# Performance work log

Measured on AMD Instinct MI355X. Metric: run time of the kernel, lower is better.

## Reference

```python
import jax, jax.numpy as jnp
import numpy as np

COMMITMENT_COST = 0.25
NUM_EMBEDDINGS = 4096
EMBEDDING_DIM = 256


def setup_inputs() -> dict:
    key = jax.random.key(0)
    kx, ke = jax.random.split(key)
    x = jax.random.normal(kx, (64, 1024, EMBEDDING_DIM), dtype=jnp.float32)
    # nn.Embedding weight initialized uniform(-1/K, 1/K)
    emb = jax.random.uniform(ke, (NUM_EMBEDDINGS, EMBEDDING_DIM), dtype=jnp.float32,
                             minval=-1.0 / NUM_EMBEDDINGS, maxval=1.0 / NUM_EMBEDDINGS)
    return {"x": x, "emb": emb}


def reference(x, emb):
    D = emb.shape[1]
    flat_x = x.reshape(-1, D)                                    # [N, D]
    distances = (jnp.sum(flat_x * flat_x, axis=1, keepdims=True)
                 - 2.0 * flat_x @ emb.T
                 + jnp.sum(emb * emb, axis=1))
    indices = jnp.argmin(distances, axis=1)                      # [N]
    quantized = emb[indices].reshape(x.shape)                    # [..., D]
    e_latent_loss = jnp.mean((jax.lax.stop_gradient(quantized) - x) ** 2)
    q_latent_loss = jnp.mean((quantized - jax.lax.stop_gradient(x)) ** 2)
    loss = q_latent_loss + COMMITMENT_COST * e_latent_loss
    # straight-through estimator
    quantized = x + jax.lax.stop_gradient(quantized - x)
    return quantized, loss, indices[:, None]
```

## Files before the change

kernel.cpp:

```cpp
#include <hip/hip_runtime.h>
#include <math.h>

#define DIMD 256
#define KCODES 4096
#define NROWS 65536
#define QN (NROWS * DIMD)

constexpr int P1_BM = 64;
constexpr int P1_BN = 128;
constexpr int NT    = KCODES / P1_BN;
constexpr int NCHUNK = NT * 2;
constexpr float TAU2 = 7.5e-4f;
constexpr float TAU2B = TAU2 + 1e-5f;
constexpr int CAP   = 48;
constexpr int NS    = 8;

typedef __attribute__((ext_vector_type(8))) short bf16x8;
typedef __attribute__((ext_vector_type(4))) float f32x4;

#define VM8() asm volatile("s_waitcnt vmcnt(8)" ::: "memory")
#define VM0() asm volatile("s_waitcnt vmcnt(0)" ::: "memory")

__device__ __forceinline__ unsigned short f2bf(float f) {
    unsigned int u = __builtin_bit_cast(unsigned int, f);
    u += 0x7fffu + ((u >> 16) & 1u);
    return (unsigned short)(u >> 16);
}

__device__ __forceinline__ float opaque(float v) {
    asm volatile("" : "+v"(v));
    return v;
}

__device__ __forceinline__ void gload_lds16(const void* g, void* l) {
    __builtin_amdgcn_global_load_lds(
        (const __attribute__((address_space(1))) unsigned int*)g,
        (__attribute__((address_space(3))) unsigned int*)l, 16, 0, 0);
}

__global__ void sx_kernel(const float* __restrict__ x, float* __restrict__ sx) {
    const int j   = threadIdx.x & 7;
    const int row = blockIdx.x * 32 + (threadIdx.x >> 3);
    const float* p = x + (size_t)row * DIMD;
    float total = 0.0f;
    #pragma unroll
    for (int half = 0; half < 2; ++half) {
        const float* b = p + half * 128;
        const float v0 = b[j];
        float r = opaque(v0 * v0);
        #pragma unroll
        for (int i = 8; i < 128; i += 8) {
            const float v = b[i + j];
            r += opaque(v * v);
        }
        const float s1  = r  + __shfl_xor(r, 1, 64);
        const float s2  = s1 + __shfl_xor(s1, 2, 64);
        const float res = s2 + __shfl_xor(s2, 4, 64);
        total = (half == 0) ? res : (total + res);
    }
    if (j == 0) sx[row] = total;
}

__global__ void se_kernel(const float* __restrict__ emb, float* __restrict__ se) {
    const int j   = threadIdx.x & 7;
    const int row = blockIdx.x * 32 + (threadIdx.x >> 3);
    const float* p = emb + (size_t)row * DIMD;
    float total = 0.0f;
    #pragma unroll
    for (int half = 0; half < 2; ++half) {
        const float* b = p + half * 128;
        const float v0 = b[j];
        float r = opaque(v0 * v0);
        #pragma unroll
        for (int i = 8; i < 128; i += 8) {
            const float v = b[i + j];
            r += opaque(v * v);
        }
        const float s1  = r  + __shfl_xor(r, 1, 64);
        const float s2  = s1 + __shfl_xor(s1, 2, 64);
        const float res = s2 + __shfl_xor(s2, 4, 64);
        total = (half == 0) ? res : (total + res);
    }
    if (j == 0) se[row] = total;
}

__global__ void conv_emb_kernel(const float* __restrict__ emb, unsigned short* __restrict__ embh) {
    const int i = blockIdx.x * blockDim.x + threadIdx.x;
    const float4 v = ((const float4*)emb)[i];
    ushort4 h;
    h.x = f2bf(v.x); h.y = f2bf(v.y); h.z = f2bf(v.z); h.w = f2bf(v.w);
    ((ushort4*)embh)[i] = h;
}

__global__ __launch_bounds__(256, 2)
void pass1_kernel(const float* __restrict__ x, const unsigned short* __restrict__ embh,
                  unsigned int* __restrict__ cand, int* __restrict__ cnt_out) {
    __shared__ unsigned short Bs[2][16384];
    __shared__ unsigned int cand_lds[P1_BM * CAP];
    __shared__ float part[4][32];
    __shared__ float tilemax[P1_BM];
    __shared__ int   cnts[P1_BM];

    const int t    = threadIdx.x;
    const int w    = t >> 6;
    const int lane = t & 63;
    const int quad = lane >> 4;
    const int lm   = lane & 15;
    const int wr   = w >> 1;
    const int wc   = w & 1;
    const int row0 = blockIdx.x * P1_BM;

    if (t < P1_BM) cnts[t] = 0;

    bf16x8 afr[2][8];
    #pragma unroll
    for (int f = 0; f < 2; ++f) {
        const float* xr = x + (size_t)(row0 + wr * 32 + f * 16 + lm) * DIMD + quad * 8;
        #pragma unroll
        for (int c = 0; c < 8; ++c) {
            const float4 v0 = *(const float4*)(xr + c * 32);
            const float4 v1 = *(const float4*)(xr + c * 32 + 4);
            bf16x8 h;
            h[0] = (short)f2bf(v0.x); h[1] = (short)f2bf(v0.y);
            h[2] = (short)f2bf(v0.z); h[3] = (short)f2bf(v0.w);
            h[4] = (short)f2bf(v1.x); h[5] = (short)f2bf(v1.y);
            h[6] = (short)f2bf(v1.z); h[7] = (short)f2bf(v1.w);
            afr[f][c] = h;
        }
    }

    auto stage = [&](int buf, int m) {
        const int c0  = (m >> 1) * P1_BN;
        const int kcb = (m & 1) * 128;
        #pragma unroll
        for (int i = 0; i < 8; ++i) {
            const int seg = i * 4 + w;
            const int c   = seg * 4 + (lane >> 4);
            const int kk  = ((lane & 15) ^ (c & 15)) * 8;
            const unsigned short* src = embh + (size_t)(c0 + c) * DIMD + kcb + kk;
            gload_lds16(src, &Bs[buf][seg * 512]);
        }
    };

    stage(0, 0);
    int buf = 0;

    float rmg[2][4];
    #pragma unroll
    for (int f = 0; f < 2; ++f)
        #pragma unroll
        for (int reg = 0; reg < 4; ++reg) rmg[f][reg] = -INFINITY;

    for (int tile = 0; tile < NT; ++tile) {
        const int c0 = tile * P1_BN;
        f32x4 acc[2][4];
        #pragma unroll
        for (int f = 0; f < 2; ++f)
            #pragma unroll
            for (int g = 0; g < 4; ++g) acc[f][g] = (f32x4){0.f, 0.f, 0.f, 0.f};

        #pragma unroll
        for (int kb = 0; kb < 2; ++kb) {
            const int m = tile * 2 + kb;
            __syncthreads();
            if (m + 1 < NCHUNK) {
                stage(buf ^ 1, m + 1);
                VM8();
            } else {
                VM0();
            }
            __syncthreads();

            #pragma unroll
            for (int ks = 0; ks < 4; ++ks) {
                bf16x8 b[4];
                #pragma unroll
                for (int g = 0; g < 4; ++g) {
                    const int c = wc * 64 + g * 16 + lm;
                    b[g] = *(const bf16x8*)
                        &Bs[buf][c * 128 + ((((ks << 2) + quad) ^ lm) << 3)];
                }
                #pragma unroll
                for (int f = 0; f < 2; ++f)
                    #pragma unroll
                    for (int g = 0; g < 4; ++g)
                        acc[f][g] = __builtin_amdgcn_mfma_f32_16x16x32_bf16(
                            afr[f][kb * 4 + ks], b[g], acc[f][g], 0, 0, 0);
            }
            buf ^= 1;
        }

        #pragma unroll
        for (int f = 0; f < 2; ++f) {
            f32x4 mm4;
            #pragma unroll
            for (int reg = 0; reg < 4; ++reg) {
                float mm = fmaxf(fmaxf(acc[f][0][reg], acc[f][1][reg]),
                                 fmaxf(acc[f][2][reg], acc[f][3][reg]));
                #pragma unroll
                for (int off = 1; off < 16; off <<= 1)
                    mm = fmaxf(mm, __shfl_xor(mm, off, 64));
                mm4[reg] = mm;
            }
            if (lm == 0)
                *(f32x4*)&part[w][f * 16 + quad * 4] = mm4;
        }

        __syncthreads();
        if (t < P1_BM) {
            const int trg = t >> 5, loc = t & 31;
            tilemax[t] = fmaxf(part[trg * 2][loc], part[trg * 2 + 1][loc]);
        }
        __syncthreads();

        #pragma unroll
        for (int f = 0; f < 2; ++f) {
            const f32x4 tm = *(const f32x4*)&tilemax[wr * 32 + f * 16 + quad * 4];
            #pragma unroll
            for (int reg = 0; reg < 4; ++reg) {
                rmg[f][reg] = fmaxf(rmg[f][reg], tm[reg]);
                const float thr = rmg[f][reg] - TAU2;
                const int r = wr * 32 + f * 16 + quad * 4 + reg;
                #pragma unroll
                for (int g = 0; g < 4; ++g) {
                    const float dv = acc[f][g][reg];
                    if (dv > thr) {
                        const int slot = atomicAdd(&cnts[r], 1);
                        if (slot < CAP) {
                            const unsigned int ub =
                                __builtin_bit_cast(unsigned int, fmaxf(dv, 0.0f));
                            cand_lds[r * CAP + slot] =
                                (ub & 0xFFFFF000u) |
                                (unsigned int)(c0 + wc * 64 + g * 16 + lm);
                        }
                    }
                }
            }
        }
    }
    __syncthreads();

    {
        const uint4* src = (const uint4*)cand_lds;
        uint4* dst = (uint4*)(cand + (size_t)row0 * CAP);
        #pragma unroll
        for (int i = 0; i < P1_BM * CAP / 4 / 256; ++i)
            dst[i * 256 + t] = src[i * 256 + t];
    }
    if (t < P1_BM) cnt_out[row0 + t] = (cnts[t] > CAP) ? -1 : cnts[t];
}

__global__ __launch_bounds__(256, 4)
void pass2_kernel(const float* __restrict__ x, const float* __restrict__ emb,
                  const float* __restrict__ sx, const float* __restrict__ se,
                  const unsigned int* __restrict__ cand, const int* __restrict__ cnt,
                  float* __restrict__ out, float* __restrict__ partial) {
    __shared__ float4 xsh[4][64];
    __shared__ float4 esh[4][NS][64];
    const int w = threadIdx.x >> 6, lane = threadIdx.x & 63;
    const int row = blockIdx.x * 4 + w;
    const int n = cnt[row];
    const unsigned int word = cand[(size_t)row * CAP + lane];
    const float sxr = sx[row];
    const float4 myx = ((const float4*)(x + (size_t)row * DIMD))[lane];
    const float4* emb4 = (const float4*)emb;

    xsh[w][lane] = myx;
    const float4* xs4 = &xsh[w][0];

    float bestd = INFINITY;
    int   bestc = 0x7fffffff;
    int   wslot = 0x7fffffff;

    if (n >= 1 && n <= CAP) {
        const float dtil = (lane < n)
            ? __builtin_bit_cast(float, word & 0xFFFFF000u) : -INFINITY;
        const int code = (int)(word & 0xFFFu);
        float mx = dtil;
        #pragma unroll
        for (int off = 1; off < 64; off <<= 1)
            mx = fmaxf(mx, __shfl_xor(mx, off, 64));
        const bool active = (lane < n) && (dtil > mx - TAU2B);
        const unsigned long long mask = __ballot(active);
        const int nact = __popcll(mask);
        const int slot = __popcll(mask & ((1ull << lane) - 1ull));
        unsigned long long mm = mask;
        const int ns = nact < NS ? nact : NS;
        for (int i = 0; i < ns; ++i) {
            const int li = __ffsll(mm) - 1;
            mm &= mm - 1;
            const int bc = __shfl(code, li, 64);
            gload_lds16(emb4 + (size_t)bc * 64 + lane, &esh[w][i][0]);
        }
        VM0();
        if (active) {
            float a = 0.0f;
            if (slot < NS) {
                const float4* ep4 = &esh[w][slot][0];
                #pragma unroll
                for (int d4 = 0; d4 < DIMD / 4; ++d4) {
                    const float4 ev = ep4[d4];
                    const float4 xv = xs4[d4];
                    a = fmaf(xv.x, ev.x, a);
                    a = fmaf(xv.y, ev.y, a);
                    a = fmaf(xv.z, ev.z, a);
                    a = fmaf(xv.w, ev.w, a);
                }
            } else {
                const float4* ep4 = emb4 + (size_t)code * 64;
                #pragma unroll
                for (int d4 = 0; d4 < DIMD / 4; ++d4) {
                    const float4 ev = ep4[d4];
                    const float4 xv = xs4[d4];
                    a = fmaf(xv.x, ev.x, a);
                    a = fmaf(xv.y, ev.y, a);
                    a = fmaf(xv.z, ev.z, a);
                    a = fmaf(xv.w, ev.w, a);
                }
            }
            const float t1 = sxr - 2.0f * a;
            bestd = t1 + se[code];
            bestc = code;
            wslot = slot;
        }
    } else {
        for (int c = lane; c < KCODES; c += 64) {
            const float* ep = emb + (size_t)c * DIMD;
            float a = 0.0f;
            for (int d4 = 0; d4 < DIMD / 4; ++d4) {
                const float4 xv = xs4[d4];
                const float4 ev = ((const float4*)ep)[d4];
                a = fmaf(xv.x, ev.x, a);
                a = fmaf(xv.y, ev.y, a);
                a = fmaf(xv.z, ev.z, a);
                a = fmaf(xv.w, ev.w, a);
            }
            const float t1 = sxr - 2.0f * a;
            const float dd = t1 + se[c];
            if (dd < bestd || (dd == bestd && c < bestc)) { bestd = dd; bestc = c; }
        }
    }
    #pragma unroll
    for (int off = 32; off > 0; off >>= 1) {
        const float od = __shfl_down(bestd, off, 64);
        const int   oc = __shfl_down(bestc, off, 64);
        const int   os = __shfl_down(wslot, off, 64);
        if (od < bestd || (od == bestd && oc < bestc)) {
            bestd = od; bestc = oc; wslot = os;
        }
    }
    bestc = __shfl(bestc, 0, 64);
    wslot = __shfl(wslot, 0, 64);

    const float4 e4 = (wslot < NS) ? esh[w][wslot][lane]
                                   : emb4[(size_t)bestc * 64 + lane];
    ((float4*)(out + (size_t)row * DIMD))[lane] = e4;
    const float dx = e4.x - myx.x, dy = e4.y - myx.y,
                dz = e4.z - myx.z, dw = e4.w - myx.w;
    float s = dx * dx + dy * dy + dz * dz + dw * dw;
    #pragma unroll
    for (int off = 32; off > 0; off >>= 1) s += __shfl_down(s, off, 64);
    if (lane == 0) {
        partial[row] = s;
        out[QN + 1 + row] = (float)bestc;
    }
}

__global__ void loss_reduce_kernel(const float* __restrict__ partial, float* __restrict__ out) {
    const int t = threadIdx.x;
    double s = 0.0;
    for (int i = t; i < NROWS; i += 256) s += (double)partial[i];
    __shared__ double tsum[256];
    tsum[t] = s;
    __syncthreads();
    #pragma unroll
    for (int off = 128; off > 0; off >>= 1) {
        if (t < off) tsum[t] += tsum[t + off];
        __syncthreads();
    }
    if (t == 0) out[QN] = (float)(tsum[0] * (1.25 / (double)QN));
}

extern "C" void kernel_launch(void* const* d_in, const int* in_sizes, int n_in,
                              void* d_out, int out_size, void* d_ws, size_t ws_size,
                              hipStream_t stream) {
    const float* x   = (const float*)d_in[0];
    const float* emb = (const float*)d_in[1];
    float* out = (float*)d_out;

    char* ws = (char*)d_ws;
    unsigned short* embh = (unsigned short*)ws;           ws += (size_t)KCODES * DIMD * 2;
    float* sx  = (float*)ws;                              ws += (size_t)NROWS * 4;
    float* se  = (float*)ws;                              ws += (size_t)KCODES * 4;
    unsigned int* cand = (unsigned int*)ws;               ws += (size_t)NROWS * CAP * 4;
    int*   cnt  = (int*)ws;                               ws += (size_t)NROWS * 4;
    float* partial = (float*)ws;

    conv_emb_kernel<<<KCODES * DIMD / 4 / 256, 256, 0, stream>>>(emb, embh);
    sx_kernel<<<NROWS / 32, 256, 0, stream>>>(x, sx);
    se_kernel<<<KCODES / 32, 256, 0, stream>>>(emb, se);
    pass1_kernel<<<NROWS / P1_BM, 256, 0, stream>>>(x, embh, cand, cnt);
    pass2_kernel<<<NROWS / 4, 256, 0, stream>>>(x, emb, sx, se, cand, cnt, out, partial);
    loss_reduce_kernel<<<1, 256, 0, stream>>>(partial, out);
}
```

Before: 744.0 us.

## Make pass2 waves process four rows with next-row prefetch and single-candidate shortcut

```diff
diff --git a/kernel.cpp b/kernel.cpp
--- a/kernel.cpp
+++ b/kernel.cpp
@@ -13,7 +13,8 @@
 constexpr float TAU2 = 7.5e-4f;
 constexpr float TAU2B = TAU2 + 1e-5f;
 constexpr int CAP   = 48;
-constexpr int NS    = 8;
+constexpr int NS    = 6;
+constexpr int P2_WAVES = 16384;
 
 typedef __attribute__((ext_vector_type(8))) short bf16x8;
 typedef __attribute__((ext_vector_type(4))) float f32x4;
@@ -256,113 +257,140 @@
                   const unsigned int* __restrict__ cand, const int* __restrict__ cnt,
                   float* __restrict__ out, float* __restrict__ partial) {
     __shared__ float4 xsh[4][64];
-    __shared__ float4 esh[4][NS][64];
+    __shared__ float4 esh[4][NS][65];
     const int w = threadIdx.x >> 6, lane = threadIdx.x & 63;
-    const int row = blockIdx.x * 4 + w;
-    const int n = cnt[row];
-    const unsigned int word = cand[(size_t)row * CAP + lane];
-    const float sxr = sx[row];
-    const float4 myx = ((const float4*)(x + (size_t)row * DIMD))[lane];
+    const int wid = blockIdx.x * 4 + w;
     const float4* emb4 = (const float4*)emb;
 
-    xsh[w][lane] = myx;
-    const float4* xs4 = &xsh[w][0];
-
-    float bestd = INFINITY;
-    int   bestc = 0x7fffffff;
-    int   wslot = 0x7fffffff;
-
-    if (n >= 1 && n <= CAP) {
-        const float dtil = (lane < n)
-            ? __builtin_bit_cast(float, word & 0xFFFFF000u) : -INFINITY;
-        const int code = (int)(word & 0xFFFu);
-        float mx = dtil;
-        #pragma unroll
-        for (int off = 1; off < 64; off <<= 1)
-            mx = fmaxf(mx, __shfl_xor(mx, off, 64));
-        const bool active = (lane < n) && (dtil > mx - TAU2B);
-        const unsigned long long mask = __ballot(active);
-        const int nact = __popcll(mask);
-        const int slot = __popcll(mask & ((1ull << lane) - 1ull));
-        unsigned long long mm = mask;
-        const int ns = nact < NS ? nact : NS;
-        for (int i = 0; i < ns; ++i) {
-            const int li = __ffsll(mm) - 1;
-            mm &= mm - 1;
-            const int bc = __shfl(code, li, 64);
-            gload_lds16(emb4 + (size_t)bc * 64 + lane, &esh[w][i][0]);
-        }
-        VM0();
-        if (active) {
-            float a = 0.0f;
-            if (slot < NS) {
-                const float4* ep4 = &esh[w][slot][0];
-                #pragma unroll
+    int          n    = cnt[wid];
+    unsigned int word = cand[(size_t)wid * CAP + lane];
+    float        sxr  = sx[wid];
+    float4       myx  = ((const float4*)(x + (size_t)wid * DIMD))[lane];
+
+    #pragma unroll
+    for (int r = 0; r < 4; ++r) {
+        const int row = wid + r * P2_WAVES;
+
+        int n2 = 0; unsigned int word2 = 0; float sxr2 = 0.0f; float4 myx2{};
+        if (r < 3) {
+            const int rn = wid + (r + 1) * P2_WAVES;
+            n2    = cnt[rn];
+            word2 = cand[(size_t)rn * CAP + lane];
+            sxr2  = sx[rn];
+            myx2  = ((const float4*)(x + (size_t)rn * DIMD))[lane];
+        }
+
+        xsh[w][lane] = myx;
+        const float4* xs4 = &xsh[w][0];
+
+        float bestd = INFINITY;
+        int   bestc = 0x7fffffff;
+        int   wslot = 0x7fffffff;
+        bool  fast  = false;
+
+        if (n >= 1 && n <= CAP) {
+            const float dtil = (lane < n)
+                ? __builtin_bit_cast(float, word & 0xFFFFF000u) : -INFINITY;
+            const int code = (int)(word & 0xFFFu);
+            float mx = dtil;
+            #pragma unroll
+            for (int off = 1; off < 64; off <<= 1)
+                mx = fmaxf(mx, __shfl_xor(mx, off, 64));
+            const bool active = (lane < n) && (dtil > mx - TAU2B);
+            const unsigned long long mask = __ballot(active);
+            const int nact = __popcll(mask);
+            if (nact == 1) {
+                const int li = __ffsll(mask) - 1;
+                bestc = __shfl(code, li, 64);
+                fast  = true;
+            } else {
+                const int slot = __popcll(mask & ((1ull << lane) - 1ull));
+                unsigned long long mm = mask;
+                const int ns = nact < NS ? nact : NS;
+                for (int i = 0; i < ns; ++i) {
+                    const int li = __ffsll(mm) - 1;
+                    mm &= mm - 1;
+                    const int bc = __shfl(code, li, 64);
+                    gload_lds16(emb4 + (size_t)bc * 64 + lane, &esh[w][i][0]);
+                }
+                VM0();
+                if (active) {
+                    float a = 0.0f;
+                    if (slot < NS) {
+                        const float4* ep4 = &esh[w][slot][0];
+                        #pragma unroll
+                        for (int d4 = 0; d4 < DIMD / 4; ++d4) {
+                            const float4 ev = ep4[d4];
+                            const float4 xv = xs4[d4];
+                            a = fmaf(xv.x, ev.x, a);
+                            a = fmaf(xv.y, ev.y, a);
+                            a = fmaf(xv.z, ev.z, a);
+                            a = fmaf(xv.w, ev.w, a);
+                        }
+                    } else {
+                        const float4* ep4 = emb4 + (size_t)code * 64;
+                        #pragma unroll
+                        for (int d4 = 0; d4 < DIMD / 4; ++d4) {
+                            const float4 ev = ep4[d4];
+                            const float4 xv = xs4[d4];
+                            a = fmaf(xv.x, ev.x, a);
+                            a = fmaf(xv.y, ev.y, a);
+                            a = fmaf(xv.z, ev.z, a);
+                            a = fmaf(xv.w, ev.w, a);
+                        }
+                    }
+                    const float t1 = sxr - 2.0f * a;
+                    bestd = t1 + se[code];
+                    bestc = code;
+                    wslot = slot;
+                }
+            }
+        } else {
+            for (int c = lane; c < KCODES; c += 64) {
+                const float* ep = emb + (size_t)c * DIMD;
+                float a = 0.0f;
                 for (int d4 = 0; d4 < DIMD / 4; ++d4) {
-                    const float4 ev = ep4[d4];
                     const float4 xv = xs4[d4];
+                    const float4 ev = ((const float4*)ep)[d4];
                     a = fmaf(xv.x, ev.x, a);
                     a = fmaf(xv.y, ev.y, a);
                     a = fmaf(xv.z, ev.z, a);
                     a = fmaf(xv.w, ev.w, a);
                 }
-            } else {
-                const float4* ep4 = emb4 + (size_t)code * 64;
-                #pragma unroll
-                for (int d4 = 0; d4 < DIMD / 4; ++d4) {
-                    const float4 ev = ep4[d4];
-                    const float4 xv = xs4[d4];
-                    a = fmaf(xv.x, ev.x, a);
-                    a = fmaf(xv.y, ev.y, a);
-                    a = fmaf(xv.z, ev.z, a);
-                    a = fmaf(xv.w, ev.w, a);
-                }
-            }
-            const float t1 = sxr - 2.0f * a;
-            bestd = t1 + se[code];
-            bestc = code;
-            wslot = slot;
-        }
-    } else {
-        for (int c = lane; c < KCODES; c += 64) {
-            const float* ep = emb + (size_t)c * DIMD;
-            float a = 0.0f;
-            for (int d4 = 0; d4 < DIMD / 4; ++d4) {
-                const float4 xv = xs4[d4];
-                const float4 ev = ((const float4*)ep)[d4];
-                a = fmaf(xv.x, ev.x, a);
-                a = fmaf(xv.y, ev.y, a);
-                a = fmaf(xv.z, ev.z, a);
-                a = fmaf(xv.w, ev.w, a);
-            }
-            const float t1 = sxr - 2.0f * a;
-            const float dd = t1 + se[c];
-            if (dd < bestd || (dd == bestd && c < bestc)) { bestd = dd; bestc = c; }
-        }
-    }
-    #pragma unroll
-    for (int off = 32; off > 0; off >>= 1) {
-        const float od = __shfl_down(bestd, off, 64);
-        const int   oc = __shfl_down(bestc, off, 64);
-        const int   os = __shfl_down(wslot, off, 64);
-        if (od < bestd || (od == bestd && oc < bestc)) {
-            bestd = od; bestc = oc; wslot = os;
-        }
-    }
-    bestc = __shfl(bestc, 0, 64);
-    wslot = __shfl(wslot, 0, 64);
-
-    const float4 e4 = (wslot < NS) ? esh[w][wslot][lane]
-                                   : emb4[(size_t)bestc * 64 + lane];
-    ((float4*)(out + (size_t)row * DIMD))[lane] = e4;
-    const float dx = e4.x - myx.x, dy = e4.y - myx.y,
-                dz = e4.z - myx.z, dw = e4.w - myx.w;
-    float s = dx * dx + dy * dy + dz * dz + dw * dw;
-    #pragma unroll
-    for (int off = 32; off > 0; off >>= 1) s += __shfl_down(s, off, 64);
-    if (lane == 0) {
-        partial[row] = s;
-        out[QN + 1 + row] = (float)bestc;
+                const float t1 = sxr - 2.0f * a;
+                const float dd = t1 + se[c];
+                if (dd < bestd || (dd == bestd && c < bestc)) { bestd = dd; bestc = c; }
+            }
+        }
+
+        if (!fast) {
+            #pragma unroll
+            for (int off = 32; off > 0; off >>= 1) {
+                const float od = __shfl_down(bestd, off, 64);
+                const int   oc = __shfl_down(bestc, off, 64);
+                const int   os = __shfl_down(wslot, off, 64);
+                if (od < bestd || (od == bestd && oc < bestc)) {
+                    bestd = od; bestc = oc; wslot = os;
+                }
+            }
+            bestc = __shfl(bestc, 0, 64);
+            wslot = __shfl(wslot, 0, 64);
+        }
+
+        const float4 e4 = (wslot < NS) ? esh[w][wslot][lane]
+                                       : emb4[(size_t)bestc * 64 + lane];
+        ((float4*)(out + (size_t)row * DIMD))[lane] = e4;
+        const float dx = e4.x - myx.x, dy = e4.y - myx.y,
+                    dz = e4.z - myx.z, dw = e4.w - myx.w;
+        float s = dx * dx + dy * dy + dz * dz + dw * dw;
+        #pragma unroll
+        for (int off = 32; off > 0; off >>= 1) s += __shfl_down(s, off, 64);
+        if (lane == 0) {
+            partial[row] = s;
+            out[QN + 1 + row] = (float)bestc;
+        }
+
+        n = n2; word = word2; sxr = sxr2; myx = myx2;
     }
 }
 
@@ -400,6 +428,6 @@
     sx_kernel<<<NROWS / 32, 256, 0, stream>>>(x, sx);
     se_kernel<<<KCODES / 32, 256, 0, stream>>>(emb, se);
     pass1_kernel<<<NROWS / P1_BM, 256, 0, stream>>>(x, embh, cand, cnt);
-    pass2_kernel<<<NROWS / 4, 256, 0, stream>>>(x, emb, sx, se, cand, cnt, out, partial);
+    pass2_kernel<<<P2_WAVES / 4, 256, 0, stream>>>(x, emb, sx, se, cand, cnt, out, partial);
     loss_reduce_kernel<<<1, 256, 0, stream>>>(partial, out);
 }
```

After: 783.5 us. 1.05x slower.

## Restructure candidate refinement: slot-major candidate layout, skip exact dot for unique survivors

Applied to the files above, without the earlier changes.

```diff
diff --git a/kernel.cpp b/kernel.cpp
--- a/kernel.cpp
+++ b/kernel.cpp
@@ -13,7 +13,6 @@
 constexpr float TAU2 = 7.5e-4f;
 constexpr float TAU2B = TAU2 + 1e-5f;
 constexpr int CAP   = 48;
-constexpr int NS    = 8;
 
 typedef __attribute__((ext_vector_type(8))) short bf16x8;
 typedef __attribute__((ext_vector_type(4))) float f32x4;
@@ -36,6 +35,10 @@
     __builtin_amdgcn_global_load_lds(
         (const __attribute__((address_space(1))) unsigned int*)g,
         (__attribute__((address_space(3))) unsigned int*)l, 16, 0, 0);
+}
+
+__device__ __forceinline__ float keyf(unsigned int w) {
+    return __builtin_bit_cast(float, w & 0xFFFFF000u);
 }
 
 __global__ void sx_kernel(const float* __restrict__ x, float* __restrict__ sx) {
@@ -241,11 +244,10 @@
     __syncthreads();
 
     {
-        const uint4* src = (const uint4*)cand_lds;
-        uint4* dst = (uint4*)(cand + (size_t)row0 * CAP);
-        #pragma unroll
-        for (int i = 0; i < P1_BM * CAP / 4 / 256; ++i)
-            dst[i * 256 + t] = src[i * 256 + t];
+        const int r = t & 63;
+        #pragma unroll
+        for (int s = t >> 6; s < CAP; s += 4)
+            cand[(size_t)s * NROWS + row0 + r] = cand_lds[r * CAP + s];
     }
     if (t < P1_BM) cnt_out[row0 + t] = (cnts[t] > CAP) ? -1 : cnts[t];
 }
@@ -255,81 +257,95 @@
                   const float* __restrict__ sx, const float* __restrict__ se,
                   const unsigned int* __restrict__ cand, const int* __restrict__ cnt,
                   float* __restrict__ out, float* __restrict__ partial) {
-    __shared__ float4 xsh[4][64];
-    __shared__ float4 esh[4][NS][64];
-    const int w = threadIdx.x >> 6, lane = threadIdx.x & 63;
-    const int row = blockIdx.x * 4 + w;
-    const int n = cnt[row];
-    const unsigned int word = cand[(size_t)row * CAP + lane];
-    const float sxr = sx[row];
-    const float4 myx = ((const float4*)(x + (size_t)row * DIMD))[lane];
-    const float4* emb4 = (const float4*)emb;
-
-    xsh[w][lane] = myx;
-    const float4* xs4 = &xsh[w][0];
-
-    float bestd = INFINITY;
-    int   bestc = 0x7fffffff;
-    int   wslot = 0x7fffffff;
-
-    if (n >= 1 && n <= CAP) {
-        const float dtil = (lane < n)
-            ? __builtin_bit_cast(float, word & 0xFFFFF000u) : -INFINITY;
-        const int code = (int)(word & 0xFFFu);
-        float mx = dtil;
-        #pragma unroll
-        for (int off = 1; off < 64; off <<= 1)
-            mx = fmaxf(mx, __shfl_xor(mx, off, 64));
-        const bool active = (lane < n) && (dtil > mx - TAU2B);
-        const unsigned long long mask = __ballot(active);
-        const int nact = __popcll(mask);
-        const int slot = __popcll(mask & ((1ull << lane) - 1ull));
-        unsigned long long mm = mask;
-        const int ns = nact < NS ? nact : NS;
-        for (int i = 0; i < ns; ++i) {
-            const int li = __ffsll(mm) - 1;
-            mm &= mm - 1;
-            const int bc = __shfl(code, li, 64);
-            gload_lds16(emb4 + (size_t)bc * 64 + lane, &esh[w][i][0]);
-        }
-        VM0();
-        if (active) {
-            float a = 0.0f;
-            if (slot < NS) {
-                const float4* ep4 = &esh[w][slot][0];
+    __shared__ int idx_lds[64];
+    __shared__ int wl[64];
+    __shared__ int ovf[64];
+    __shared__ int counts[2];
+    const int t = threadIdx.x;
+    const int w = t >> 6, lane = t & 63;
+    const int row0 = blockIdx.x * 64;
+
+    if (t < 2) counts[t] = 0;
+    __syncthreads();
+
+    if (t < 64) {
+        const int row = row0 + t;
+        const int n = cnt[row];
+        if (n < 0) {
+            ovf[atomicAdd(&counts[1], 1)] = t;
+        } else {
+            unsigned int kw[16];
+            #pragma unroll
+            for (int s = 0; s < 16; ++s)
+                kw[s] = cand[(size_t)s * NROWS + row];
+            float mx = -INFINITY;
+            #pragma unroll
+            for (int s = 0; s < 16; ++s)
+                if (s < n) mx = fmaxf(mx, keyf(kw[s]));
+            for (int s = 16; s < n; ++s)
+                mx = fmaxf(mx, keyf(cand[(size_t)s * NROWS + row]));
+            const float thr = mx - TAU2B;
+            int nsurv = 0, scode = 0;
+            #pragma unroll
+            for (int s = 0; s < 16; ++s)
+                if (s < n && keyf(kw[s]) > thr) { ++nsurv; scode = (int)(kw[s] & 0xFFFu); }
+            for (int s = 16; s < n; ++s) {
+                const unsigned int wd = cand[(size_t)s * NROWS + row];
+                if (keyf(wd) > thr) { ++nsurv; scode = (int)(wd & 0xFFFu); }
+            }
+            if (nsurv == 1) idx_lds[t] = scode;
+            else            wl[atomicAdd(&counts[0], 1)] = t;
+        }
+    }
+    __syncthreads();
+    const int nwl = counts[0], novf = counts[1];
+
+    if (t < nwl) {
+        const int lr = wl[t];
+        const int row = row0 + lr;
+        const int n = cnt[row];
+        const float sxr = sx[row];
+        float mx = -INFINITY;
+        for (int s = 0; s < n; ++s)
+            mx = fmaxf(mx, keyf(cand[(size_t)s * NROWS + row]));
+        const float thr = mx - TAU2B;
+        float bestd = INFINITY; int bestc = 0x7fffffff;
+        const float4* xp4 = (const float4*)(x + (size_t)row * DIMD);
+        for (int s = 0; s < n; ++s) {
+            const unsigned int wd = cand[(size_t)s * NROWS + row];
+            if (keyf(wd) > thr) {
+                const int code = (int)(wd & 0xFFFu);
+                const float4* ep4 = (const float4*)(emb + (size_t)code * DIMD);
+                float a = 0.0f;
                 #pragma unroll
                 for (int d4 = 0; d4 < DIMD / 4; ++d4) {
+                    const float4 xv = xp4[d4];
                     const float4 ev = ep4[d4];
-                    const float4 xv = xs4[d4];
                     a = fmaf(xv.x, ev.x, a);
                     a = fmaf(xv.y, ev.y, a);
                     a = fmaf(xv.z, ev.z, a);
                     a = fmaf(xv.w, ev.w, a);
                 }
-            } else {
-                const float4* ep4 = emb4 + (size_t)code * 64;
-                #pragma unroll
-                for (int d4 = 0; d4 < DIMD / 4; ++d4) {
-                    const float4 ev = ep4[d4];
-                    const float4 xv = xs4[d4];
-                    a = fmaf(xv.x, ev.x, a);
-                    a = fmaf(xv.y, ev.y, a);
-                    a = fmaf(xv.z, ev.z, a);
-                    a = fmaf(xv.w, ev.w, a);
-                }
-            }
-            const float t1 = sxr - 2.0f * a;
-            bestd = t1 + se[code];
-            bestc = code;
-            wslot = slot;
-        }
-    } else {
+                const float t1 = sxr - 2.0f * a;
+                const float dd = t1 + se[code];
+                if (dd < bestd || (dd == bestd && code < bestc)) { bestd = dd; bestc = code; }
+            }
+        }
+        idx_lds[lr] = bestc;
+    }
+
+    for (int i = w; i < novf; i += 4) {
+        const int lr = ovf[i];
+        const int row = row0 + lr;
+        const float sxr = sx[row];
+        const float4* xp4 = (const float4*)(x + (size_t)row * DIMD);
+        float bestd = INFINITY; int bestc = 0x7fffffff;
         for (int c = lane; c < KCODES; c += 64) {
-            const float* ep = emb + (size_t)c * DIMD;
+            const float4* ep4 = (const float4*)(emb + (size_t)c * DIMD);
             float a = 0.0f;
             for (int d4 = 0; d4 < DIMD / 4; ++d4) {
-                const float4 xv = xs4[d4];
-                const float4 ev = ((const float4*)ep)[d4];
+                const float4 xv = xp4[d4];
+                const float4 ev = ep4[d4];
                 a = fmaf(xv.x, ev.x, a);
                 a = fmaf(xv.y, ev.y, a);
                 a = fmaf(xv.z, ev.z, a);
@@ -339,30 +355,31 @@
             const float dd = t1 + se[c];
             if (dd < bestd || (dd == bestd && c < bestc)) { bestd = dd; bestc = c; }
         }
-    }
-    #pragma unroll
-    for (int off = 32; off > 0; off >>= 1) {
-        const float od = __shfl_down(bestd, off, 64);
-        const int   oc = __shfl_down(bestc, off, 64);
-        const int   os = __shfl_down(wslot, off, 64);
-        if (od < bestd || (od == bestd && oc < bestc)) {
-            bestd = od; bestc = oc; wslot = os;
-        }
-    }
-    bestc = __shfl(bestc, 0, 64);
-    wslot = __shfl(wslot, 0, 64);
-
-    const float4 e4 = (wslot < NS) ? esh[w][wslot][lane]
-                                   : emb4[(size_t)bestc * 64 + lane];
-    ((float4*)(out + (size_t)row * DIMD))[lane] = e4;
-    const float dx = e4.x - myx.x, dy = e4.y - myx.y,
-                dz = e4.z - myx.z, dw = e4.w - myx.w;
-    float s = dx * dx + dy * dy + dz * dz + dw * dw;
-    #pragma unroll
-    for (int off = 32; off > 0; off >>= 1) s += __shfl_down(s, off, 64);
-    if (lane == 0) {
-        partial[row] = s;
-        out[QN + 1 + row] = (float)bestc;
+        #pragma unroll
+        for (int off = 32; off > 0; off >>= 1) {
+            const float od = __shfl_down(bestd, off, 64);
+            const int   oc = __shfl_down(bestc, off, 64);
+            if (od < bestd || (od == bestd && oc < bestc)) { bestd = od; bestc = oc; }
+        }
+        if (lane == 0) idx_lds[lr] = bestc;
+    }
+    __syncthreads();
+
+    for (int r = w; r < 64; r += 4) {
+        const int row = row0 + r;
+        const int code = idx_lds[r];
+        const float4 xv = ((const float4*)(x + (size_t)row * DIMD))[lane];
+        const float4 ev = ((const float4*)(emb + (size_t)code * DIMD))[lane];
+        ((float4*)(out + (size_t)row * DIMD))[lane] = ev;
+        const float dx = ev.x - xv.x, dy = ev.y - xv.y,
+                    dz = ev.z - xv.z, dw = ev.w - xv.w;
+        float s = dx * dx + dy * dy + dz * dz + dw * dw;
+        #pragma unroll
+        for (int off = 32; off > 0; off >>= 1) s += __shfl_down(s, off, 64);
+        if (lane == 0) {
+            partial[row] = s;
+            out[QN + 1 + row] = (float)code;
+        }
     }
 }
 
@@ -400,6 +417,6 @@
     sx_kernel<<<NROWS / 32, 256, 0, stream>>>(x, sx);
     se_kernel<<<KCODES / 32, 256, 0, stream>>>(emb, se);
     pass1_kernel<<<NROWS / P1_BM, 256, 0, stream>>>(x, embh, cand, cnt);
-    pass2_kernel<<<NROWS / 4, 256, 0, stream>>>(x, emb, sx, se, cand, cnt, out, partial);
+    pass2_kernel<<<NROWS / 64, 256, 0, stream>>>(x, emb, sx, se, cand, cnt, out, partial);
     loss_reduce_kernel<<<1, 256, 0, stream>>>(partial, out);
 }
```

After: 898.3 us. +20.7%, slower.
